# Kernel tuning notes

Measured on AMD Instinct MI355X. Metric: run time of the kernel, lower is better.

Reference implementation:

```python
import jax, jax.numpy as jnp
import numpy as np

HID = 5120
NH = 40
HD = HID // NH  # 128
S = 2048        # q_len == model_max_length (prefill)


def setup_inputs() -> dict:
    key = jax.random.key(0)
    k1, k2, k3 = jax.random.split(key, 3)
    hidden_states = jax.random.normal(k1, (1, S, HID), dtype=jnp.float32)
    W_pack_w = jax.random.normal(k2, (3 * HID, HID), dtype=jnp.float32) * 0.02
    o_proj_w = jax.random.normal(k3, (HID, HID), dtype=jnp.float32) * 0.02
    k_cache = jnp.zeros((1, NH, S, HD), dtype=jnp.float32)
    v_cache = jnp.zeros((1, NH, S, HD), dtype=jnp.float32)
    input_pos = jnp.arange(S, dtype=jnp.int32)
    # persistent causal mask [bsz, 1, max_len, max_len]; True = attend
    attention_mask = jnp.tril(jnp.ones((S, S), dtype=bool))[None, None, :, :]
    return {
        "hidden_states": hidden_states,
        "W_pack_w": W_pack_w,
        "o_proj_w": o_proj_w,
        "k_cache": k_cache,
        "v_cache": v_cache,
        "input_pos": input_pos,
        "attention_mask": attention_mask,
    }


def reference(hidden_states, W_pack_w, o_proj_w, k_cache, v_cache, input_pos, attention_mask):
    bsz, q_len, _ = hidden_states.shape
    # fused QKV projection (torch Linear weight is [out, in])
    proj = jnp.einsum("bsh,oh->bso", hidden_states, W_pack_w)  # [1,S,3H]
    q, k, v = jnp.split(proj, 3, axis=-1)
    def to_heads(t):
        return t.reshape(bsz, q_len, NH, HD).transpose(0, 2, 1, 3)  # [1,NH,S,HD]
    q, k, v = to_heads(q), to_heads(k), to_heads(v)
    # KV-cache scatter update at input_pos
    k_cache = k_cache.at[:, :, input_pos, :].set(k)
    v_cache = v_cache.at[:, :, input_pos, :].set(v)
    # s_len = input_pos[-1] + 1 == S (full prefill, static shape)
    keys = k_cache  # [1,NH,S,HD]
    vals = v_cache
    mask = attention_mask[:, :, input_pos, :]  # [1,1,S,S]
    scale = 1.0 / jnp.sqrt(jnp.asarray(HD, dtype=q.dtype))
    scores = jnp.einsum("bhqd,bhkd->bhqk", q, keys) * scale  # [1,NH,S,S]
    neg = jnp.finfo(scores.dtype).min
    scores = jnp.where(mask, scores, neg)
    attn = jax.nn.softmax(scores, axis=-1)
    out = jnp.einsum("bhqk,bhkd->bhqd", attn, vals)  # [1,NH,S,HD]
    out = out.transpose(0, 2, 1, 3).reshape(bsz, q_len, HID)
    return jnp.einsum("bsh,oh->bso", out, o_proj_w)
```

## Files before the change

### kernel.cpp

```cpp
#include <hip/hip_runtime.h>

#define S 2048
#define HID 5120
#define NH 40
#define HD 128

typedef unsigned short u16;
typedef __attribute__((ext_vector_type(8))) short short8;
typedef __attribute__((ext_vector_type(4))) float f32x4;

__device__ __forceinline__ u16 f2bf(float f) {
  union { float f; unsigned u; } x; x.f = f;
  unsigned r = x.u + 0x7fffu + ((x.u >> 16) & 1u);
  return (u16)(r >> 16);
}

__device__ __forceinline__ void gl_lds16(const void* g, void* l) {
  __builtin_amdgcn_global_load_lds((__attribute__((address_space(1))) void*)g,
                                   (__attribute__((address_space(3))) void*)l,
                                   16, 0, 0);
}

__global__ __launch_bounds__(256) void cvt4(const float4* __restrict__ s,
                                            ushort4* __restrict__ d, int n4) {
  int i = blockIdx.x * 256 + threadIdx.x;
  if (i >= n4) return;
  float4 v = s[i];
  ushort4 o;
  o.x = f2bf(v.x); o.y = f2bf(v.y); o.z = f2bf(v.z); o.w = f2bf(v.w);
  d[i] = o;
}

__global__ __launch_bounds__(256) void gemm_bt(
    const u16* __restrict__ A, const u16* __restrict__ B,
    int N, int K,
    float* __restrict__ C,
    u16* __restrict__ qb, u16* __restrict__ kb, u16* __restrict__ vtb,
    int mode)
{
  __shared__ __align__(16) u16 As[128 * 64];
  __shared__ __align__(16) u16 Bs[128 * 64];
  const int tid = threadIdx.x;
  const int lane = tid & 63;
  const int wid = tid >> 6;
  const int wm = wid >> 1, wn = wid & 1;
  const int l16 = lane & 15, quad = lane >> 4;
  const int m0 = blockIdx.x * 128, n0 = blockIdx.y * 128;

  f32x4 acc[4][4];
#pragma unroll
  for (int i = 0; i < 4; ++i)
#pragma unroll
    for (int j = 0; j < 4; ++j)
      acc[i][j] = (f32x4){0.f, 0.f, 0.f, 0.f};

  const int srow = lane >> 3;
  const int scb = lane & 7;

  for (int k0 = 0; k0 < K; k0 += 64) {
#pragma unroll
    for (int cc = 0; cc < 4; ++cc) {
      int c = wid * 4 + cc;
      int row = c * 8 + srow;
      int cb = scb ^ (row & 7);
      gl_lds16(A + (long)(m0 + row) * K + k0 + cb * 8, &As[c * 512]);
    }
#pragma unroll
    for (int cc = 0; cc < 4; ++cc) {
      int c = wid * 4 + cc;
      int row = c * 8 + srow;
      int cb = scb ^ (row & 7);
      gl_lds16(B + (long)(n0 + row) * K + k0 + cb * 8, &Bs[c * 512]);
    }
    __syncthreads();
#pragma unroll
    for (int kk = 0; kk < 64; kk += 32) {
      short8 af[4], bg[4];
      const int cb0 = (kk >> 3) + quad;
#pragma unroll
      for (int i = 0; i < 4; ++i) {
        int row = wm * 64 + i * 16 + l16;
        af[i] = *(const short8*)&As[row * 64 + (cb0 ^ (row & 7)) * 8];
      }
#pragma unroll
      for (int j = 0; j < 4; ++j) {
        int row = wn * 64 + j * 16 + l16;
        bg[j] = *(const short8*)&Bs[row * 64 + (cb0 ^ (row & 7)) * 8];
      }
#pragma unroll
      for (int i = 0; i < 4; ++i)
#pragma unroll
        for (int j = 0; j < 4; ++j)
          acc[i][j] = __builtin_amdgcn_mfma_f32_16x16x32_bf16(af[i], bg[j], acc[i][j], 0, 0, 0);
    }
    __syncthreads();
  }

  if (mode == 0) {
#pragma unroll
    for (int i = 0; i < 4; ++i)
#pragma unroll
      for (int r = 0; r < 4; ++r) {
        int row = m0 + wm * 64 + i * 16 + quad * 4 + r;
#pragma unroll
        for (int j = 0; j < 4; ++j) {
          int col = n0 + wn * 64 + j * 16 + l16;
          C[(long)row * N + col] = acc[i][j][r];
        }
      }
  } else {
    const int which = n0 / HID;
    const int head = (n0 % HID) >> 7;
    const float qs = 0.08838834764831845f;
#pragma unroll
    for (int i = 0; i < 4; ++i)
#pragma unroll
      for (int j = 0; j < 4; ++j)
#pragma unroll
        for (int r = 0; r < 4; ++r) {
          int sI = m0 + wm * 64 + i * 16 + quad * 4 + r;
          int d = wn * 64 + j * 16 + l16;
          float v = acc[i][j][r];
          if (which == 0)      qb[((long)head * S + sI) * HD + d] = f2bf(v * qs);
          else if (which == 1) kb[((long)head * S + sI) * HD + d] = f2bf(v);
          else                 vtb[((long)head * HD + d) * S + sI] = f2bf(v);
        }
  }
}

__global__ __launch_bounds__(256) void attn_kernel(
    const u16* __restrict__ qg, const u16* __restrict__ kg,
    const u16* __restrict__ vg, u16* __restrict__ og)
{
  __shared__ __align__(16) u16 Qs[64 * 128];
  __shared__ __align__(16) u16 Ks[64 * 128];
  __shared__ __align__(16) u16 Vs[128 * 64];
  __shared__ float redm[2][64];
  __shared__ float reds[2][64];

  const int tid = threadIdx.x;
  const int lane = tid & 63;
  const int wid = tid >> 6;
  const int wm = wid >> 1, wn = wid & 1;
  const int l16 = lane & 15, quad = lane >> 4;
  const int qt = blockIdx.x;
  const int h = blockIdx.y;
  const int q0 = qt * 64;

  u16* Ps = Ks;

  {
    const u16* src = qg + ((long)h * S + q0) * HD;
#pragma unroll
    for (int cc = 0; cc < 4; ++cc) {
      int c = wid * 4 + cc;
      int row = c * 4 + (lane >> 4);
      int cb = (lane & 15) ^ (row & 7);
      gl_lds16(src + row * HD + cb * 8, &Qs[c * 512]);
    }
  }

  f32x4 acc_o[2][4];
#pragma unroll
  for (int i = 0; i < 2; ++i)
#pragma unroll
    for (int j = 0; j < 4; ++j)
      acc_o[i][j] = (f32x4){0.f, 0.f, 0.f, 0.f};
  float m_st[2][4], l_st[2][4];
#pragma unroll
  for (int i = 0; i < 2; ++i)
#pragma unroll
    for (int r = 0; r < 4; ++r) { m_st[i][r] = -1e30f; l_st[i][r] = 0.f; }

  for (int kt = 0; kt <= qt; ++kt) {
    __syncthreads();
    {
      const u16* ksrc = kg + ((long)h * S + kt * 64) * HD;
#pragma unroll
      for (int cc = 0; cc < 4; ++cc) {
        int c = wid * 4 + cc;
        int row = c * 4 + (lane >> 4);
        int cb = (lane & 15) ^ (row & 7);
        gl_lds16(ksrc + row * HD + cb * 8, &Ks[c * 512]);
      }
      const u16* vsrc = vg + (long)h * HD * S + kt * 64;
#pragma unroll
      for (int cc = 0; cc < 4; ++cc) {
        int c = wid * 4 + cc;
        int row = c * 8 + (lane >> 3);
        int cb = (lane & 7) ^ (row & 7);
        gl_lds16(vsrc + (long)row * S + cb * 8, &Vs[c * 512]);
      }
    }
    __syncthreads();

    f32x4 acc_s[2][2];
#pragma unroll
    for (int i = 0; i < 2; ++i)
#pragma unroll
      for (int j = 0; j < 2; ++j)
        acc_s[i][j] = (f32x4){0.f, 0.f, 0.f, 0.f};
#pragma unroll
    for (int kk = 0; kk < 128; kk += 32) {
      short8 aq[2], bk[2];
      const int cb0 = (kk >> 3) + quad;
#pragma unroll
      for (int i = 0; i < 2; ++i) {
        int row = wm * 32 + i * 16 + l16;
        aq[i] = *(const short8*)&Qs[row * 128 + (cb0 ^ (row & 7)) * 8];
      }
#pragma unroll
      for (int j = 0; j < 2; ++j) {
        int row = wn * 32 + j * 16 + l16;
        bk[j] = *(const short8*)&Ks[row * 128 + (cb0 ^ (row & 7)) * 8];
      }
#pragma unroll
      for (int i = 0; i < 2; ++i)
#pragma unroll
        for (int j = 0; j < 2; ++j)
          acc_s[i][j] = __builtin_amdgcn_mfma_f32_16x16x32_bf16(aq[i], bk[j], acc_s[i][j], 0, 0, 0);
    }

    if (kt == qt) {
#pragma unroll
      for (int i = 0; i < 2; ++i)
#pragma unroll
        for (int j = 0; j < 2; ++j)
#pragma unroll
          for (int r = 0; r < 4; ++r) {
            int row = wm * 32 + i * 16 + quad * 4 + r;
            int col = wn * 32 + j * 16 + l16;
            if (col > row) acc_s[i][j][r] = -1e30f;
          }
    }

#pragma unroll
    for (int i = 0; i < 2; ++i)
#pragma unroll
      for (int r = 0; r < 4; ++r) {
        float v = fmaxf(acc_s[i][0][r], acc_s[i][1][r]);
        v = fmaxf(v, __shfl_xor(v, 1));
        v = fmaxf(v, __shfl_xor(v, 2));
        v = fmaxf(v, __shfl_xor(v, 4));
        v = fmaxf(v, __shfl_xor(v, 8));
        if (l16 == 0) redm[wn][wm * 32 + i * 16 + quad * 4 + r] = v;
      }
    __syncthreads();

    float alpha[2][4], mnew[2][4], psum[2][4];
#pragma unroll
    for (int i = 0; i < 2; ++i)
#pragma unroll
      for (int r = 0; r < 4; ++r) {
        int row = wm * 32 + i * 16 + quad * 4 + r;
        float mn = fmaxf(m_st[i][r], fmaxf(redm[0][row], redm[1][row]));
        mnew[i][r] = mn;
        alpha[i][r] = __expf(m_st[i][r] - mn);
        m_st[i][r] = mn;
        psum[i][r] = 0.f;
      }
#pragma unroll
    for (int i = 0; i < 2; ++i)
#pragma unroll
      for (int j = 0; j < 2; ++j)
#pragma unroll
        for (int r = 0; r < 4; ++r) {
          int row = wm * 32 + i * 16 + quad * 4 + r;
          int col = wn * 32 + j * 16 + l16;
          float p = __expf(acc_s[i][j][r] - mnew[i][r]);
          psum[i][r] += p;
          Ps[row * 64 + ((col >> 3) ^ (row & 7)) * 8 + (col & 7)] = f2bf(p);
        }
#pragma unroll
    for (int i = 0; i < 2; ++i)
#pragma unroll
      for (int r = 0; r < 4; ++r) {
        float v = psum[i][r];
        v += __shfl_xor(v, 1);
        v += __shfl_xor(v, 2);
        v += __shfl_xor(v, 4);
        v += __shfl_xor(v, 8);
        if (l16 == 0) reds[wn][wm * 32 + i * 16 + quad * 4 + r] = v;
      }
    __syncthreads();

#pragma unroll
    for (int i = 0; i < 2; ++i)
#pragma unroll
      for (int r = 0; r < 4; ++r) {
        int row = wm * 32 + i * 16 + quad * 4 + r;
        l_st[i][r] = alpha[i][r] * l_st[i][r] + reds[0][row] + reds[1][row];
#pragma unroll
        for (int j = 0; j < 4; ++j)
          acc_o[i][j][r] *= alpha[i][r];
      }
#pragma unroll
    for (int kk = 0; kk < 64; kk += 32) {
      short8 ap[2], bv[4];
      const int cb0 = (kk >> 3) + quad;
#pragma unroll
      for (int i = 0; i < 2; ++i) {
        int m = wm * 32 + i * 16 + l16;
        ap[i] = *(const short8*)&Ps[m * 64 + (cb0 ^ (m & 7)) * 8];
      }
#pragma unroll
      for (int j = 0; j < 4; ++j) {
        int n = wn * 64 + j * 16 + l16;
        bv[j] = *(const short8*)&Vs[n * 64 + (cb0 ^ (n & 7)) * 8];
      }
#pragma unroll
      for (int i = 0; i < 2; ++i)
#pragma unroll
        for (int j = 0; j < 4; ++j)
          acc_o[i][j] = __builtin_amdgcn_mfma_f32_16x16x32_bf16(ap[i], bv[j], acc_o[i][j], 0, 0, 0);
    }
  }

#pragma unroll
  for (int i = 0; i < 2; ++i)
#pragma unroll
    for (int r = 0; r < 4; ++r) {
      int row = wm * 32 + i * 16 + quad * 4 + r;
      float inv = 1.f / l_st[i][r];
#pragma unroll
      for (int j = 0; j < 4; ++j) {
        int d = wn * 64 + j * 16 + l16;
        og[(long)(q0 + row) * HID + h * HD + d] = f2bf(acc_o[i][j][r] * inv);
      }
    }
}

extern "C" void kernel_launch(void* const* d_in, const int* in_sizes, int n_in,
                              void* d_out, int out_size, void* d_ws, size_t ws_size,
                              hipStream_t stream) {
  const float* hs = (const float*)d_in[0];
  const float* wp = (const float*)d_in[1];
  const float* wo = (const float*)d_in[2];
  float* out = (float*)d_out;
  char* ws = (char*)d_ws;

  u16* hsb = (u16*)(ws);
  u16* wpb = (u16*)(ws + 20971520L);
  u16* wob = (u16*)(ws + 178257920L);
  u16* qb  = (u16*)(ws + 230686720L);
  u16* kb  = (u16*)(ws + 251658240L);
  u16* vtb = (u16*)(ws + 272629760L);
  u16* aob = (u16*)(ws + 293601280L);
  if (ws_size < 314572800UL) return;

  cvt4<<<10240, 256, 0, stream>>>((const float4*)hs, (ushort4*)hsb, 2621440);
  cvt4<<<76800, 256, 0, stream>>>((const float4*)wp, (ushort4*)wpb, 19660800);
  cvt4<<<25600, 256, 0, stream>>>((const float4*)wo, (ushort4*)wob, 6553600);

  gemm_bt<<<dim3(16, 120), 256, 0, stream>>>(hsb, wpb, 15360, 5120,
                                             nullptr, qb, kb, vtb, 1);
  attn_kernel<<<dim3(32, 40), 256, 0, stream>>>(qb, kb, vtb, aob);
  gemm_bt<<<dim3(16, 40), 256, 0, stream>>>(aob, wob, 5120, 5120,
                                            out, nullptr, nullptr, nullptr, 0);
}
```

Measured before the change: 1.657 ms.

## Replace GEMM with 256x256-tile, 8-wave, double-buffered pipelined kernel

Replaces the 128x128 single-buffered GEMM with a 256x256 tile kernel using 512 threads and double-buffered LDS. Global-to-LDS loads for later k-steps are interleaved with MFMA groups under explicit vmcnt waits, barriers and setprio hints. The aim is to hide load latency and raise data reuse per tile in both projection GEMMs. In exchange it uses 128KB of LDS per block and more accumulator registers, which caps occupancy, and the hand-written pipeline is fragile.

After: 1.556 ms. 6.1% less time.

```diff
diff --git a/kernel.cpp b/kernel.cpp
--- a/kernel.cpp
+++ b/kernel.cpp
@@ -31,101 +31,183 @@
   d[i] = o;
 }
 
-__global__ __launch_bounds__(256) void gemm_bt(
+__global__ __launch_bounds__(512, 2) void gemm256(
     const u16* __restrict__ A, const u16* __restrict__ B,
     int N, int K,
     float* __restrict__ C,
     u16* __restrict__ qb, u16* __restrict__ kb, u16* __restrict__ vtb,
     int mode)
 {
-  __shared__ __align__(16) u16 As[128 * 64];
-  __shared__ __align__(16) u16 Bs[128 * 64];
+  __shared__ __align__(16) u16 As[2][16384];
+  __shared__ __align__(16) u16 Bs[2][16384];
+
   const int tid = threadIdx.x;
   const int lane = tid & 63;
-  const int wid = tid >> 6;
-  const int wm = wid >> 1, wn = wid & 1;
+  const int wave = tid >> 6;
+  const int wm = wave >> 2, wn = wave & 3;
   const int l16 = lane & 15, quad = lane >> 4;
-  const int m0 = blockIdx.x * 128, n0 = blockIdx.y * 128;
-
-  f32x4 acc[4][4];
-#pragma unroll
-  for (int i = 0; i < 4; ++i)
-#pragma unroll
-    for (int j = 0; j < 4; ++j)
-      acc[i][j] = (f32x4){0.f, 0.f, 0.f, 0.f};
-
-  const int srow = lane >> 3;
-  const int scb = lane & 7;
-
-  for (int k0 = 0; k0 < K; k0 += 64) {
-#pragma unroll
-    for (int cc = 0; cc < 4; ++cc) {
-      int c = wid * 4 + cc;
-      int row = c * 8 + srow;
-      int cb = scb ^ (row & 7);
-      gl_lds16(A + (long)(m0 + row) * K + k0 + cb * 8, &As[c * 512]);
-    }
-#pragma unroll
-    for (int cc = 0; cc < 4; ++cc) {
-      int c = wid * 4 + cc;
-      int row = c * 8 + srow;
-      int cb = scb ^ (row & 7);
-      gl_lds16(B + (long)(n0 + row) * K + k0 + cb * 8, &Bs[c * 512]);
-    }
-    __syncthreads();
-#pragma unroll
-    for (int kk = 0; kk < 64; kk += 32) {
-      short8 af[4], bg[4];
-      const int cb0 = (kk >> 3) + quad;
-#pragma unroll
-      for (int i = 0; i < 4; ++i) {
-        int row = wm * 64 + i * 16 + l16;
-        af[i] = *(const short8*)&As[row * 64 + (cb0 ^ (row & 7)) * 8];
-      }
-#pragma unroll
-      for (int j = 0; j < 4; ++j) {
-        int row = wn * 64 + j * 16 + l16;
-        bg[j] = *(const short8*)&Bs[row * 64 + (cb0 ^ (row & 7)) * 8];
-      }
-#pragma unroll
-      for (int i = 0; i < 4; ++i)
-#pragma unroll
-        for (int j = 0; j < 4; ++j)
-          acc[i][j] = __builtin_amdgcn_mfma_f32_16x16x32_bf16(af[i], bg[j], acc[i][j], 0, 0, 0);
-    }
-    __syncthreads();
-  }
+
+  const int m0 = (blockIdx.x & 7) << 8;
+  const int n0 = (blockIdx.x >> 3) << 8;
+
+  const int srow = wave * 8 + (lane >> 3);
+  const int scb  = (lane & 7) ^ ((lane >> 3) & 7);
+  const u16* Abase = A + (long)(m0 + srow) * K + scb * 8;
+  const u16* Bbase = B + (long)(n0 + srow) * K + scb * 8;
+  u16* AsW = &As[0][0] + wave * 512;
+  u16* BsW = &Bs[0][0] + wave * 512;
+
+  const u16* ArBase = &As[0][0] + (wm * 128 + l16) * 64;
+  const u16* BrBase = &Bs[0][0] + (wn * 64 + l16) * 64;
+  const int acb0 = ((quad) ^ (l16 & 7)) * 8;
+  const int acb1 = ((4 + quad) ^ (l16 & 7)) * 8;
+
+  f32x4 acc[8][4];
+#pragma unroll
+  for (int i = 0; i < 8; ++i)
+#pragma unroll
+    for (int j = 0; j < 4; ++j) acc[i][j] = (f32x4){0.f, 0.f, 0.f, 0.f};
+
+  short8 aP[2][2], aN[2][2], brg[4][2];
+
+  const int nt = K >> 6;
+
+#define STAGE_A(bufi, h, kt) do {                                         \
+    const u16* g_ = Abase + (long)(h) * 128 * K + (long)(kt) * 64;        \
+    gl_lds16(g_,           AsW + (bufi) * 16384 + (h) * 8192);            \
+    gl_lds16(g_ + 64L * K, AsW + (bufi) * 16384 + (h) * 8192 + 4096);     \
+  } while (0)
+
+#define STAGE_B(bufi, h, kt) do {                                         \
+    const u16* g_ = Bbase + (long)(h) * 128 * K + (long)(kt) * 64;        \
+    gl_lds16(g_,           BsW + (bufi) * 16384 + (h) * 8192);            \
+    gl_lds16(g_ + 64L * K, BsW + (bufi) * 16384 + (h) * 8192 + 4096);     \
+  } while (0)
+
+#define RD_A(dst, bufi, q) do {                                           \
+    const u16* p_ = ArBase + (bufi) * 16384 + (q) * 2048;                 \
+    dst[0][0] = *(const short8*)(p_ + acb0);                              \
+    dst[0][1] = *(const short8*)(p_ + acb1);                              \
+    dst[1][0] = *(const short8*)(p_ + 1024 + acb0);                       \
+    dst[1][1] = *(const short8*)(p_ + 1024 + acb1);                       \
+  } while (0)
+
+#define RD_B(bufi) do {                                                   \
+    const u16* p_ = BrBase + (bufi) * 16384;                              \
+    brg[0][0] = *(const short8*)(p_ + acb0);                              \
+    brg[0][1] = *(const short8*)(p_ + acb1);                              \
+    brg[1][0] = *(const short8*)(p_ + 1024 + acb0);                       \
+    brg[1][1] = *(const short8*)(p_ + 1024 + acb1);                       \
+    brg[2][0] = *(const short8*)(p_ + 2048 + acb0);                       \
+    brg[2][1] = *(const short8*)(p_ + 2048 + acb1);                       \
+    brg[3][0] = *(const short8*)(p_ + 3072 + acb0);                       \
+    brg[3][1] = *(const short8*)(p_ + 3072 + acb1);                       \
+  } while (0)
+
+#define MFMA1(mi, j, ar) do {                                                             \
+    acc[mi][j] = __builtin_amdgcn_mfma_f32_16x16x32_bf16(ar[0], brg[j][0], acc[mi][j], 0, 0, 0); \
+    acc[mi][j] = __builtin_amdgcn_mfma_f32_16x16x32_bf16(ar[1], brg[j][1], acc[mi][j], 0, 0, 0); \
+  } while (0)
+
+#define MFMA_Q(q, a) do {                                                 \
+    MFMA1((q)*2 + 0, 0, a[0]); MFMA1((q)*2 + 0, 1, a[0]);                 \
+    MFMA1((q)*2 + 0, 2, a[0]); MFMA1((q)*2 + 0, 3, a[0]);                 \
+    MFMA1((q)*2 + 1, 0, a[1]); MFMA1((q)*2 + 1, 1, a[1]);                 \
+    MFMA1((q)*2 + 1, 2, a[1]); MFMA1((q)*2 + 1, 3, a[1]);                 \
+  } while (0)
+
+#define ASM_VMCNT(n) asm volatile("s_waitcnt vmcnt(" #n ")" ::: "memory")
+#define BAR() __builtin_amdgcn_s_barrier()
+#define PRIO1 __builtin_amdgcn_s_setprio(1)
+#define PRIO0 __builtin_amdgcn_s_setprio(0)
+
+#define KGROUP(S1, S2, VMN) do {                                          \
+    const int bi = t & 1, bn = bi ^ 1;                                    \
+                                                                 \
+    RD_B(bi);                                                             \
+    RD_A(aN, bi, 1);                                                      \
+    if (S1) STAGE_A(bn, 1, t + 1);                                        \
+    BAR();                                                                \
+    PRIO1; MFMA_Q(0, aP); PRIO0;                                          \
+    BAR();                                                                \
+                                                                 \
+    RD_A(aP, bi, 2);                                                      \
+    if (S2) STAGE_B(bi, 0, t + 2);                                        \
+    BAR();                                                                \
+    PRIO1; MFMA_Q(1, aN); PRIO0;                                          \
+    BAR();                                                                \
+                                                                 \
+    RD_A(aN, bi, 3);                                                      \
+    if (S2) STAGE_B(bi, 1, t + 2);                                        \
+    BAR();                                                                \
+    PRIO1; MFMA_Q(2, aP); PRIO0;                                          \
+    BAR();                                                                \
+                                                                 \
+    ASM_VMCNT(VMN);                                                       \
+    __builtin_amdgcn_sched_barrier(0);                                    \
+    BAR();                                                                \
+    if (S1) RD_A(aP, bn, 0);                                              \
+    PRIO1; MFMA_Q(3, aN); PRIO0;                                          \
+    if (S2) STAGE_A(bi, 0, t + 2);                                        \
+    BAR();                                                                \
+  } while (0)
+
+  STAGE_A(0, 0, 0); STAGE_A(0, 1, 0);
+  STAGE_B(0, 0, 0); STAGE_B(0, 1, 0);
+  STAGE_B(1, 0, 1); STAGE_B(1, 1, 1);
+  ASM_VMCNT(4);
+  __builtin_amdgcn_sched_barrier(0);
+  BAR();
+  STAGE_A(1, 0, 1);
+  RD_A(aP, 0, 0);
+
+  for (int t = 0; t < nt - 2; ++t) { KGROUP(1, 1, 4); }
+  { int t = nt - 2; KGROUP(1, 0, 0); }
+  { int t = nt - 1; KGROUP(0, 0, 0); }
 
   if (mode == 0) {
 #pragma unroll
-    for (int i = 0; i < 4; ++i)
+    for (int mi = 0; mi < 8; ++mi)
 #pragma unroll
       for (int r = 0; r < 4; ++r) {
-        int row = m0 + wm * 64 + i * 16 + quad * 4 + r;
-#pragma unroll
-        for (int j = 0; j < 4; ++j) {
-          int col = n0 + wn * 64 + j * 16 + l16;
-          C[(long)row * N + col] = acc[i][j][r];
-        }
+        int row = m0 + wm * 128 + mi * 16 + quad * 4 + r;
+        float* cp = C + (long)row * N + n0 + wn * 64 + l16;
+#pragma unroll
+        for (int j = 0; j < 4; ++j) cp[j * 16] = acc[mi][j][r];
       }
   } else {
     const int which = n0 / HID;
-    const int head = (n0 % HID) >> 7;
+    const int hbase = (n0 % HID) >> 7;
     const float qs = 0.08838834764831845f;
 #pragma unroll
-    for (int i = 0; i < 4; ++i)
-#pragma unroll
-      for (int j = 0; j < 4; ++j)
+    for (int mi = 0; mi < 8; ++mi)
+#pragma unroll
+      for (int j = 0; j < 4; ++j) {
+        int colIn = wn * 64 + j * 16 + l16;
+        int head = hbase + (colIn >> 7);
+        int d = colIn & 127;
 #pragma unroll
         for (int r = 0; r < 4; ++r) {
-          int sI = m0 + wm * 64 + i * 16 + quad * 4 + r;
-          int d = wn * 64 + j * 16 + l16;
-          float v = acc[i][j][r];
+          int sI = m0 + wm * 128 + mi * 16 + quad * 4 + r;
+          float v = acc[mi][j][r];
           if (which == 0)      qb[((long)head * S + sI) * HD + d] = f2bf(v * qs);
           else if (which == 1) kb[((long)head * S + sI) * HD + d] = f2bf(v);
           else                 vtb[((long)head * HD + d) * S + sI] = f2bf(v);
         }
+      }
   }
+
+#undef STAGE_A
+#undef STAGE_B
+#undef RD_A
+#undef RD_B
+#undef MFMA1
+#undef MFMA_Q
+#undef ASM_VMCNT
+#undef BAR
+#undef PRIO1
+#undef PRIO0
+#undef KGROUP
 }
 
 __global__ __launch_bounds__(256) void attn_kernel(
@@ -352,9 +434,9 @@
   cvt4<<<76800, 256, 0, stream>>>((const float4*)wp, (ushort4*)wpb, 19660800);
   cvt4<<<25600, 256, 0, stream>>>((const float4*)wo, (ushort4*)wob, 6553600);
 
-  gemm_bt<<<dim3(16, 120), 256, 0, stream>>>(hsb, wpb, 15360, 5120,
-                                             nullptr, qb, kb, vtb, 1);
+  gemm256<<<dim3(480), dim3(512), 0, stream>>>(hsb, wpb, 15360, 5120,
+                                               nullptr, qb, kb, vtb, 1);
   attn_kernel<<<dim3(32, 40), 256, 0, stream>>>(qb, kb, vtb, aob);
-  gemm_bt<<<dim3(16, 40), 256, 0, stream>>>(aob, wob, 5120, 5120,
-                                            out, nullptr, nullptr, nullptr, 0);
-}
+  gemm256<<<dim3(160), dim3(512), 0, stream>>>(aob, wob, 5120, 5120,
+                                               out, nullptr, nullptr, nullptr, 0);
+}
```
